# Kernel tuning notes

Hardware: AMD Instinct MI355X
Metric: run time of the kernel (lower is better)

## Reference

```python
import jax, jax.numpy as jnp
import numpy as np

N_BONDS = 50000
N_EDGES = 600000
BOND_DIM = 64
SPH_DIM = 64
UNITS = 64


def setup_inputs() -> dict:
    key = jax.random.key(0)
    k1, k2, k3, k4, k5 = jax.random.split(key, 5)
    bond_features = jax.random.normal(k1, (N_BONDS, BOND_DIM), dtype=jnp.float32)
    edges_sph_features = jax.random.normal(k2, (N_EDGES, SPH_DIM), dtype=jnp.float32)
    # column 0: sorted segment ids (tf.math.segment_sum requires sorted ids)
    seg = jnp.sort(jax.random.randint(k3, (N_EDGES,), 0, N_BONDS, dtype=jnp.int32))
    nbr = jax.random.randint(k4, (N_EDGES,), 0, N_BONDS, dtype=jnp.int32)
    edges_neighbor = jnp.stack([seg, nbr], axis=1)  # [n_edges, 2]
    kernel = jax.random.normal(k5, (BOND_DIM + SPH_DIM, UNITS), dtype=jnp.float32) * 0.05
    bias = jnp.zeros((UNITS,), dtype=jnp.float32)
    return {
        "bond_features": bond_features,
        "edges_sph_features": edges_sph_features,
        "edges_neighbor": edges_neighbor,
        "kernel": kernel,
        "bias": bias,
    }


def reference(bond_features, edges_sph_features, edges_neighbor, kernel, bias):
    # gather bond features of the neighboring bond for each edge (line-graph)
    gathered = bond_features[edges_neighbor[:, 1]]            # [E, bond_dim]
    concated = jnp.concatenate([gathered, edges_sph_features], axis=-1)  # [E, bond_dim+sph_dim]
    # scatter-reduce into segments (sorted ids; fixed num_segments for jit)
    aggregated = jax.ops.segment_sum(
        concated, edges_neighbor[:, 0], num_segments=N_BONDS,
        indices_are_sorted=True,
    )  # [n_bonds, bond_dim+sph_dim]
    return aggregated @ kernel + bias
```

## Files before the change

kernel.cpp:

```cpp
#include <hip/hip_runtime.h>

#define N_BONDS 50000
#define N_EDGES 600000
#define R_BONDS 8
#define WAVES_PER_BLOCK 4
#define BONDS_PER_BLOCK (R_BONDS * WAVES_PER_BLOCK)

typedef float f4 __attribute__((ext_vector_type(4)));

__device__ __forceinline__ float bcastf(float v, int l) {
    return __builtin_bit_cast(float, __builtin_amdgcn_readlane(__builtin_bit_cast(int, v), l));
}

__global__ __launch_bounds__(256)
void fill_starts(const int* __restrict__ edges, int* __restrict__ starts) {
    const int e = blockIdx.x * blockDim.x + threadIdx.x;
    if (e >= N_EDGES) return;
    const int2* edges2 = (const int2*)edges;
    const int s  = edges2[e].x;
    const int sp = (e == 0) ? -1 : edges2[e - 1].x;
    for (int b = sp + 1; b <= s; ++b) starts[b] = e;
    if (e == N_EDGES - 1)
        for (int b = s + 1; b <= N_BONDS; ++b) starts[b] = N_EDGES;
}

__global__ __launch_bounds__(256, 6)
void fused_gather_segsum_mm(const float* __restrict__ bond,
                            const float* __restrict__ sph,
                            const int*   __restrict__ edges,
                            const float* __restrict__ Kmat,
                            const float* __restrict__ bias,
                            const int*   __restrict__ starts,
                            float* __restrict__ out)
{
    __shared__ float ldsK[128 * 64];
    const int tid  = threadIdx.x;
    const int lane = tid & 63;
    const int wid  = tid >> 6;

    {
        const f4* K4 = (const f4*)Kmat;
        f4*       L4 = (f4*)ldsK;
        #pragma unroll
        for (int i = 0; i < 8; ++i) L4[tid + i * 256] = K4[tid + i * 256];
    }
    __syncthreads();

    const int b0 = blockIdx.x * BONDS_PER_BLOCK + wid * R_BONDS;
    if (b0 >= N_BONDS) return;

    int st[R_BONDS + 1];
    #pragma unroll
    for (int r = 0; r <= R_BONDS; ++r)
        st[r] = __builtin_amdgcn_readfirstlane(starts[b0 + r]);

    float slotG[R_BONDS], slotS[R_BONDS];

    #pragma unroll
    for (int r = 0; r < R_BONDS; ++r) {
        float aG = 0.f, aS = 0.f;
        int e = st[r];
        const int t = st[r + 1];

        for (; e + 4 <= t; e += 4) {
            const int n0 = edges[2 * e + 1];
            const int n1 = edges[2 * e + 3];
            const int n2 = edges[2 * e + 5];
            const int n3 = edges[2 * e + 7];
            const float g0 = bond[n0 * 64 + lane];
            const float g1 = bond[n1 * 64 + lane];
            const float g2 = bond[n2 * 64 + lane];
            const float g3 = bond[n3 * 64 + lane];
            const float s0 = __builtin_nontemporal_load(&sph[(e + 0) * 64 + lane]);
            const float s1 = __builtin_nontemporal_load(&sph[(e + 1) * 64 + lane]);
            const float s2 = __builtin_nontemporal_load(&sph[(e + 2) * 64 + lane]);
            const float s3 = __builtin_nontemporal_load(&sph[(e + 3) * 64 + lane]);
            aG += (g0 + g1) + (g2 + g3);
            aS += (s0 + s1) + (s2 + s3);
        }
        for (; e < t; ++e) {
            const int n = edges[2 * e + 1];
            aG += bond[n * 64 + lane];
            aS += __builtin_nontemporal_load(&sph[e * 64 + lane]);
        }
        slotG[r] = aG;
        slotS[r] = aS;
    }

    float acc[R_BONDS];
    const float bl = bias[lane];
    #pragma unroll
    for (int r = 0; r < R_BONDS; ++r) acc[r] = bl;

    #pragma unroll 2
    for (int d = 0; d < 64; ++d) {
        const float kt = ldsK[d * 64 + lane];
        const float kb = ldsK[(64 + d) * 64 + lane];
        #pragma unroll
        for (int r = 0; r < R_BONDS; ++r) {
            acc[r] = fmaf(bcastf(slotG[r], d), kt, acc[r]);
            acc[r] = fmaf(bcastf(slotS[r], d), kb, acc[r]);
        }
    }

    #pragma unroll
    for (int r = 0; r < R_BONDS; ++r)
        if (b0 + r < N_BONDS)
            __builtin_nontemporal_store(acc[r], &out[(b0 + r) * 64 + lane]);
}

extern "C" void kernel_launch(void* const* d_in, const int* in_sizes, int n_in,
                              void* d_out, int out_size, void* d_ws, size_t ws_size,
                              hipStream_t stream) {
    const float* bond  = (const float*)d_in[0];
    const float* sph   = (const float*)d_in[1];
    const int*   edges = (const int*)d_in[2];
    const float* Kmat  = (const float*)d_in[3];
    const float* bias  = (const float*)d_in[4];
    float* out   = (float*)d_out;
    int* starts  = (int*)d_ws;

    fill_starts<<<(N_EDGES + 255) / 256, 256, 0, stream>>>(edges, starts);

    const int nblocks = (N_BONDS + BONDS_PER_BLOCK - 1) / BONDS_PER_BLOCK;
    fused_gather_segsum_mm<<<nblocks, 256, 0, stream>>>(bond, sph, edges, Kmat,
                                                        bias, starts, out);
}
```

Measured before the change: 88.74 us.

## Process four edges per wave with float4 loads and flattened segment walk

Rewrites the gather/segment-sum loop so each wave walks the flattened edge range of its 8 bonds. Each 16-lane subgroup loads a full 64-float row with float4 loads, so one instruction covers four edges. Edge indices are loaded once per 64-edge window and broadcast by shuffle. Segment boundaries are handled with masked accumulation and a cross-subgroup shuffle reduction. This is meant to cut per-edge load instruction count and the short serial per-bond loops, at the cost of more shuffle and branch overhead and a lower occupancy hint.

```diff
diff --git a/kernel.cpp b/kernel.cpp
--- a/kernel.cpp
+++ b/kernel.cpp
@@ -3,13 +3,17 @@
 #define N_BONDS 50000
 #define N_EDGES 600000
 #define R_BONDS 8
-#define WAVES_PER_BLOCK 4
-#define BONDS_PER_BLOCK (R_BONDS * WAVES_PER_BLOCK)
+#define BONDS_PER_BLOCK 32
 
 typedef float f4 __attribute__((ext_vector_type(4)));
 
 __device__ __forceinline__ float bcastf(float v, int l) {
     return __builtin_bit_cast(float, __builtin_amdgcn_readlane(__builtin_bit_cast(int, v), l));
+}
+__device__ __forceinline__ f4 f4zero() { return (f4){0.f, 0.f, 0.f, 0.f}; }
+__device__ __forceinline__ void fma4(f4& a, float s, const f4& b) {
+    a.x = fmaf(s, b.x, a.x); a.y = fmaf(s, b.y, a.y);
+    a.z = fmaf(s, b.z, a.z); a.w = fmaf(s, b.w, a.w);
 }
 
 __global__ __launch_bounds__(256)
@@ -24,7 +28,7 @@
         for (int b = s + 1; b <= N_BONDS; ++b) starts[b] = N_EDGES;
 }
 
-__global__ __launch_bounds__(256, 6)
+__global__ __launch_bounds__(256, 4)
 void fused_gather_segsum_mm(const float* __restrict__ bond,
                             const float* __restrict__ sph,
                             const int*   __restrict__ edges,
@@ -37,6 +41,8 @@
     const int tid  = threadIdx.x;
     const int lane = tid & 63;
     const int wid  = tid >> 6;
+    const int fl   = lane & 15;
+    const int sg   = lane >> 4;
 
     {
         const f4* K4 = (const f4*)Kmat;
@@ -54,59 +60,114 @@
     for (int r = 0; r <= R_BONDS; ++r)
         st[r] = __builtin_amdgcn_readfirstlane(starts[b0 + r]);
 
+    const int eb    = st[0];
+    const int total = st[R_BONDS] - eb;
+
+    const f4*   bond4  = (const f4*)bond;
+    const f4*   sph4   = (const f4*)sph;
+    const int2* edges2 = (const int2*)edges;
+
     float slotG[R_BONDS], slotS[R_BONDS];
+    f4 aG = f4zero(), aS = f4zero();
+    int r = 0, cs = 0, bnd = st[1] - eb;
 
-    #pragma unroll
-    for (int r = 0; r < R_BONDS; ++r) {
-        float aG = 0.f, aS = 0.f;
-        int e = st[r];
-        const int t = st[r + 1];
+    auto txr = [&](f4 v) -> float {
+        v.x += __shfl_xor(v.x, 16); v.y += __shfl_xor(v.y, 16);
+        v.z += __shfl_xor(v.z, 16); v.w += __shfl_xor(v.w, 16);
+        v.x += __shfl_xor(v.x, 32); v.y += __shfl_xor(v.y, 32);
+        v.z += __shfl_xor(v.z, 32); v.w += __shfl_xor(v.w, 32);
+        const int src = lane >> 2;
+        const float s0 = __shfl(v.x, src), s1 = __shfl(v.y, src);
+        const float s2 = __shfl(v.z, src), s3 = __shfl(v.w, src);
+        const float r01 = (lane & 1) ? s1 : s0;
+        const float r23 = (lane & 1) ? s3 : s2;
+        return (lane & 2) ? r23 : r01;
+    };
 
-        for (; e + 4 <= t; e += 4) {
-            const int n0 = edges[2 * e + 1];
-            const int n1 = edges[2 * e + 3];
-            const int n2 = edges[2 * e + 5];
-            const int n3 = edges[2 * e + 7];
-            const float g0 = bond[n0 * 64 + lane];
-            const float g1 = bond[n1 * 64 + lane];
-            const float g2 = bond[n2 * 64 + lane];
-            const float g3 = bond[n3 * 64 + lane];
-            const float s0 = __builtin_nontemporal_load(&sph[(e + 0) * 64 + lane]);
-            const float s1 = __builtin_nontemporal_load(&sph[(e + 1) * 64 + lane]);
-            const float s2 = __builtin_nontemporal_load(&sph[(e + 2) * 64 + lane]);
-            const float s3 = __builtin_nontemporal_load(&sph[(e + 3) * 64 + lane]);
-            aG += (g0 + g1) + (g2 + g3);
-            aS += (s0 + s1) + (s2 + s3);
+    auto slowpath = [&](int q, f4 GV, f4 SV) {
+        const int qe = q + sg;
+        while (true) {
+            const float m = (qe >= cs && qe < bnd) ? 1.f : 0.f;
+            fma4(aG, m, GV); fma4(aS, m, SV);
+            if (bnd > q + 4) break;
+            const float tG = txr(aG), tS = txr(aS);
+            #pragma unroll
+            for (int rr = 0; rr < R_BONDS; ++rr)
+                if (rr == r) { slotG[rr] = tG; slotS[rr] = tS; }
+            aG = f4zero(); aS = f4zero();
+            cs = bnd;
+            ++r;
+            if (r >= R_BONDS) { bnd = 0x7fffffff; break; }
+            #pragma unroll
+            for (int rr = 2; rr <= R_BONDS; ++rr)
+                if (r + 1 == rr) bnd = st[rr] - eb;
         }
-        for (; e < t; ++e) {
-            const int n = edges[2 * e + 1];
-            aG += bond[n * 64 + lane];
-            aS += __builtin_nontemporal_load(&sph[e * 64 + lane]);
+    };
+
+    int w0 = 0;
+    while (w0 < total) {
+        int wlen = total - w0; if (wlen > 64) wlen = 64;
+        int2 p = make_int2(0, 0);
+        if (lane < wlen) p = edges2[eb + w0 + lane];
+        const int ng = (wlen + 3) >> 2;
+
+        for (int c = 0; c < ng; c += 4) {
+            f4 g0, g1, g2, g3, s0, s1, s2, s3;
+
+#define ISSUE(GG, GV, SV) do { \
+            if ((c + GG) < ng) { \
+                const int idx_ = (c + GG) * 4 + sg; \
+                const int nbr_ = __shfl(p.y, idx_); \
+                int qe_ = w0 + idx_; if (qe_ >= total) qe_ = total - 1; \
+                GV = bond4[nbr_ * 16 + fl]; \
+                SV = __builtin_nontemporal_load(&sph4[(eb + qe_) * 16 + fl]); \
+            } else { GV = f4zero(); SV = f4zero(); } } while (0)
+
+            ISSUE(0, g0, s0); ISSUE(1, g1, s1); ISSUE(2, g2, s2); ISSUE(3, g3, s3);
+#undef ISSUE
+
+#define ACCG(GG, GV, SV) do { \
+            if ((c + GG) < ng) { \
+                const int q_ = w0 + (c + GG) * 4; \
+                if (q_ + 4 <= bnd) { aG += GV; aS += SV; } \
+                else slowpath(q_, GV, SV); \
+            } } while (0)
+
+            ACCG(0, g0, s0); ACCG(1, g1, s1); ACCG(2, g2, s2); ACCG(3, g3, s3);
+#undef ACCG
         }
-        slotG[r] = aG;
-        slotS[r] = aS;
+        w0 += wlen;
+    }
+
+    {
+        const float tG = txr(aG), tS = txr(aS);
+        #pragma unroll
+        for (int rr = 0; rr < R_BONDS; ++rr) {
+            if (rr == r)     { slotG[rr] = tG;  slotS[rr] = tS; }
+            else if (rr > r) { slotG[rr] = 0.f; slotS[rr] = 0.f; }
+        }
     }
 
     float acc[R_BONDS];
     const float bl = bias[lane];
     #pragma unroll
-    for (int r = 0; r < R_BONDS; ++r) acc[r] = bl;
+    for (int rr = 0; rr < R_BONDS; ++rr) acc[rr] = bl;
 
     #pragma unroll 2
     for (int d = 0; d < 64; ++d) {
         const float kt = ldsK[d * 64 + lane];
         const float kb = ldsK[(64 + d) * 64 + lane];
         #pragma unroll
-        for (int r = 0; r < R_BONDS; ++r) {
-            acc[r] = fmaf(bcastf(slotG[r], d), kt, acc[r]);
-            acc[r] = fmaf(bcastf(slotS[r], d), kb, acc[r]);
+        for (int rr = 0; rr < R_BONDS; ++rr) {
+            acc[rr] = fmaf(bcastf(slotG[rr], d), kt, acc[rr]);
+            acc[rr] = fmaf(bcastf(slotS[rr], d), kb, acc[rr]);
         }
     }
 
     #pragma unroll
-    for (int r = 0; r < R_BONDS; ++r)
-        if (b0 + r < N_BONDS)
-            __builtin_nontemporal_store(acc[r], &out[(b0 + r) * 64 + lane]);
+    for (int rr = 0; rr < R_BONDS; ++rr)
+        if (b0 + rr < N_BONDS)
+            __builtin_nontemporal_store(acc[rr], &out[(b0 + rr) * 64 + lane]);
 }
 
 extern "C" void kernel_launch(void* const* d_in, const int* in_sizes, int n_in,
@@ -117,8 +178,8 @@
     const int*   edges = (const int*)d_in[2];
     const float* Kmat  = (const float*)d_in[3];
     const float* bias  = (const float*)d_in[4];
-    float* out   = (float*)d_out;
-    int* starts  = (int*)d_ws;
+    float* out  = (float*)d_out;
+    int* starts = (int*)d_ws;
 
     fill_starts<<<(N_EDGES + 255) / 256, 256, 0, stream>>>(edges, starts);
 
```

After: 79.60 us. 1.11x faster.

## Vectorize edge gather with float4 per quarter-wave and software pipelining

Applied to the files above, without the earlier changes.

Each wave now splits into four 16-lane groups. Each group loads a full 64-float row as float4, so one wave handles four edges per step. Loads are double-buffered across iterations and the partial sums are reduced across groups with shuffles. The block grows to 512 threads with 4 bonds per wave, which targets better memory-level parallelism and wider loads. The cost is extra shuffle reduction work and masked work on partially filled edge quads.

```diff
diff --git a/kernel.cpp b/kernel.cpp
--- a/kernel.cpp
+++ b/kernel.cpp
@@ -2,14 +2,19 @@
 
 #define N_BONDS 50000
 #define N_EDGES 600000
-#define R_BONDS 8
-#define WAVES_PER_BLOCK 4
-#define BONDS_PER_BLOCK (R_BONDS * WAVES_PER_BLOCK)
+#define R_BONDS 4
+#define THREADS 512
+#define BONDS_PER_BLOCK 32
 
 typedef float f4 __attribute__((ext_vector_type(4)));
 
 __device__ __forceinline__ float bcastf(float v, int l) {
     return __builtin_bit_cast(float, __builtin_amdgcn_readlane(__builtin_bit_cast(int, v), l));
+}
+__device__ __forceinline__ f4 f4zero() { return (f4){0.f, 0.f, 0.f, 0.f}; }
+__device__ __forceinline__ void fma4(f4& a, float s, const f4& b) {
+    a.x = fmaf(s, b.x, a.x); a.y = fmaf(s, b.y, a.y);
+    a.z = fmaf(s, b.z, a.z); a.w = fmaf(s, b.w, a.w);
 }
 
 __global__ __launch_bounds__(256)
@@ -24,7 +29,7 @@
         for (int b = s + 1; b <= N_BONDS; ++b) starts[b] = N_EDGES;
 }
 
-__global__ __launch_bounds__(256, 6)
+__global__ __launch_bounds__(THREADS, 8)
 void fused_gather_segsum_mm(const float* __restrict__ bond,
                             const float* __restrict__ sph,
                             const int*   __restrict__ edges,
@@ -37,12 +42,14 @@
     const int tid  = threadIdx.x;
     const int lane = tid & 63;
     const int wid  = tid >> 6;
+    const int fl   = lane & 15;
+    const int sg   = lane >> 4;
 
     {
         const f4* K4 = (const f4*)Kmat;
         f4*       L4 = (f4*)ldsK;
         #pragma unroll
-        for (int i = 0; i < 8; ++i) L4[tid + i * 256] = K4[tid + i * 256];
+        for (int i = 0; i < 4; ++i) L4[tid + i * THREADS] = K4[tid + i * THREADS];
     }
     __syncthreads();
 
@@ -54,45 +61,73 @@
     for (int r = 0; r <= R_BONDS; ++r)
         st[r] = __builtin_amdgcn_readfirstlane(starts[b0 + r]);
 
+    const f4* bond4 = (const f4*)bond;
+    const f4* sph4  = (const f4*)sph;
+
+    auto txr = [&](f4 v) -> float {
+        v.x += __shfl_xor(v.x, 16); v.y += __shfl_xor(v.y, 16);
+        v.z += __shfl_xor(v.z, 16); v.w += __shfl_xor(v.w, 16);
+        v.x += __shfl_xor(v.x, 32); v.y += __shfl_xor(v.y, 32);
+        v.z += __shfl_xor(v.z, 32); v.w += __shfl_xor(v.w, 32);
+        const int src = lane >> 2;
+        const float s0 = __shfl(v.x, src), s1 = __shfl(v.y, src);
+        const float s2 = __shfl(v.z, src), s3 = __shfl(v.w, src);
+        const float r01 = (lane & 1) ? s1 : s0;
+        const float r23 = (lane & 1) ? s3 : s2;
+        return (lane & 2) ? r23 : r01;
+    };
+
+    auto loadq = [&](int ea, f4& gv, f4& sv) {
+        const int e0 = (ea     < N_EDGES) ? ea     : N_EDGES - 1;
+        const int e1 = (ea + 1 < N_EDGES) ? ea + 1 : N_EDGES - 1;
+        const int e2 = (ea + 2 < N_EDGES) ? ea + 2 : N_EDGES - 1;
+        const int e3 = (ea + 3 < N_EDGES) ? ea + 3 : N_EDGES - 1;
+        const int n0 = edges[2 * e0 + 1];
+        const int n1 = edges[2 * e1 + 1];
+        const int n2 = edges[2 * e2 + 1];
+        const int n3 = edges[2 * e3 + 1];
+        const int ns = (sg == 0) ? n0 : (sg == 1) ? n1 : (sg == 2) ? n2 : n3;
+        const int es = (sg == 0) ? e0 : (sg == 1) ? e1 : (sg == 2) ? e2 : e3;
+        gv = bond4[ns * 16 + fl];
+        sv = __builtin_nontemporal_load(&sph4[es * 16 + fl]);
+    };
+    auto accq = [&](int ea, int t, const f4& gv, const f4& sv, f4& aG, f4& aS) {
+        const float sel = (ea + sg < t) ? 1.f : 0.f;
+        fma4(aG, sel, gv);
+        fma4(aS, sel, sv);
+    };
+
+    auto run_bond = [&](int s, int t, float& oG, float& oS) {
+        f4 aG = f4zero(), aS = f4zero();
+        const int nq = (t - s + 3) >> 2;
+        if (nq > 0) {
+            f4 gA, sA, gB, sB;
+            loadq(s, gA, sA);
+            int q = 0;
+            for (; q + 2 <= nq; q += 2) {
+                loadq(s + 4 * (q + 1), gB, sB);
+                accq(s + 4 * q, t, gA, sA, aG, aS);
+                if (q + 2 < nq) loadq(s + 4 * (q + 2), gA, sA);
+                accq(s + 4 * (q + 1), t, gB, sB, aG, aS);
+            }
+            if (q < nq) accq(s + 4 * q, t, gA, sA, aG, aS);
+        }
+        oG = txr(aG);
+        oS = txr(aS);
+    };
+
     float slotG[R_BONDS], slotS[R_BONDS];
-
-    #pragma unroll
-    for (int r = 0; r < R_BONDS; ++r) {
-        float aG = 0.f, aS = 0.f;
-        int e = st[r];
-        const int t = st[r + 1];
-
-        for (; e + 4 <= t; e += 4) {
-            const int n0 = edges[2 * e + 1];
-            const int n1 = edges[2 * e + 3];
-            const int n2 = edges[2 * e + 5];
-            const int n3 = edges[2 * e + 7];
-            const float g0 = bond[n0 * 64 + lane];
-            const float g1 = bond[n1 * 64 + lane];
-            const float g2 = bond[n2 * 64 + lane];
-            const float g3 = bond[n3 * 64 + lane];
-            const float s0 = __builtin_nontemporal_load(&sph[(e + 0) * 64 + lane]);
-            const float s1 = __builtin_nontemporal_load(&sph[(e + 1) * 64 + lane]);
-            const float s2 = __builtin_nontemporal_load(&sph[(e + 2) * 64 + lane]);
-            const float s3 = __builtin_nontemporal_load(&sph[(e + 3) * 64 + lane]);
-            aG += (g0 + g1) + (g2 + g3);
-            aS += (s0 + s1) + (s2 + s3);
-        }
-        for (; e < t; ++e) {
-            const int n = edges[2 * e + 1];
-            aG += bond[n * 64 + lane];
-            aS += __builtin_nontemporal_load(&sph[e * 64 + lane]);
-        }
-        slotG[r] = aG;
-        slotS[r] = aS;
-    }
+    run_bond(st[0], st[1], slotG[0], slotS[0]);
+    run_bond(st[1], st[2], slotG[1], slotS[1]);
+    run_bond(st[2], st[3], slotG[2], slotS[2]);
+    run_bond(st[3], st[4], slotG[3], slotS[3]);
 
     float acc[R_BONDS];
     const float bl = bias[lane];
     #pragma unroll
     for (int r = 0; r < R_BONDS; ++r) acc[r] = bl;
 
-    #pragma unroll 2
+    #pragma unroll 4
     for (int d = 0; d < 64; ++d) {
         const float kt = ldsK[d * 64 + lane];
         const float kb = ldsK[(64 + d) * 64 + lane];
@@ -117,12 +152,12 @@
     const int*   edges = (const int*)d_in[2];
     const float* Kmat  = (const float*)d_in[3];
     const float* bias  = (const float*)d_in[4];
-    float* out   = (float*)d_out;
-    int* starts  = (int*)d_ws;
+    float* out  = (float*)d_out;
+    int* starts = (int*)d_ws;
 
     fill_starts<<<(N_EDGES + 255) / 256, 256, 0, stream>>>(edges, starts);
 
     const int nblocks = (N_BONDS + BONDS_PER_BLOCK - 1) / BONDS_PER_BLOCK;
-    fused_gather_segsum_mm<<<nblocks, 256, 0, stream>>>(bond, sph, edges, Kmat,
-                                                        bias, starts, out);
+    fused_gather_segsum_mm<<<nblocks, THREADS, 0, stream>>>(bond, sph, edges, Kmat,
+                                                            bias, starts, out);
 }
```

New measurement: 77.72 us. 1.14x faster.
